# Optimization experiments

Measured on AMD Instinct MI355X. Metric: run time of the kernel, lower is better.

The kernel has to match this reference:

```python
import jax, jax.numpy as jnp
import numpy as np
from jax import lax

B, H, W, C = 4, 1024, 1024, 16


def setup_inputs() -> dict:
    key = jax.random.key(0)
    k1, k2 = jax.random.split(key)
    feat = jax.random.normal(k1, (B, H, W, C), dtype=jnp.float32)
    mask = jax.random.randint(k2, (B, H, W), 0, 2).astype(bool)
    return {"feat": feat, "mask": mask}


def _sum_pool(f, m):
    """Minkowski sum pooling, kernel 3, stride 2, dilation 1, dim 2.

    Output coord c exists iff any input coord in {2c, 2c+1}^2 is occupied
    (floor(coord/2) strided coordinate map). Output feature at c sums input
    features at 2c + {-1,0,1}^2 (3x3 window centered on the strided coord).
    """
    f = f * m[..., None].astype(f.dtype)  # zero features at empty coords
    # 3x3 sum window, stride 2, pad 1 -> output spatial dims H//2, W//2
    out = lax.reduce_window(
        f, jnp.zeros((), f.dtype), lax.add,
        window_dimensions=(1, 3, 3, 1),
        window_strides=(1, 2, 2, 1),
        padding=((0, 0), (1, 1), (1, 1), (0, 0)),
    )
    b, h, w = m.shape
    m2 = m.reshape(b, h // 2, 2, w // 2, 2).any(axis=(2, 4))  # strided coord map
    out = out * m2[..., None].astype(out.dtype)  # keep only occupied outputs
    return out, m2


def reference(feat, mask):
    c1, m1 = _sum_pool(feat, mask)
    c2, m2 = _sum_pool(c1, m1)
    c3, m3 = _sum_pool(c2, m2)
    return (c2, c3)
```

## Files before the change

kernel.cpp:

```cpp
#include <hip/hip_runtime.h>


constexpr int Hh = 1024, Ww = 1024;
constexpr int TW3 = 16, TH3 = 8;
constexpr int NU = 4 * TW3 + 3;
constexpr int NV = 2 * TW3 + 1;
constexpr int NY = TW3;
constexpr int NTH = 320;

#define BARRIER_LDS() asm volatile("s_waitcnt lgkmcnt(0)\ns_barrier" ::: "memory")

__device__ inline float4 add3(const float4& a, const float4& b, const float4& c) {
    return make_float4(a.x + b.x + c.x, a.y + b.y + c.y,
                       a.z + b.z + c.z, a.w + b.w + c.w);
}

__global__ __launch_bounds__(NTH) void fused3(
    const float* __restrict__ featp, const int* __restrict__ maskp,
    float4* __restrict__ c2o, float4* __restrict__ c3o)
{
    const int j = blockIdx.x;
    const int k = blockIdx.y;
    const int b = blockIdx.z;
    const int P0 = TW3 * j, Q0 = TH3 * k;
    const int F0 = 8 * P0 - 7;
    const int T0 = 8 * Q0 - 7;

    const int tid = threadIdx.x;
    const int c4 = tid & 3;
    const int u  = tid >> 2;
    const bool aAct = tid < NU * 4;
    const bool vAct = tid < NV * 4;
    const bool yAct = tid < NY * 4;

    __shared__ float4 c1m[2][NU][5];
    __shared__ float4 c2mS[2][NV][5];
    __shared__ unsigned char m1L[2][NU];
    __shared__ unsigned char m2L[2][NV];

    const float4* feat4 = reinterpret_cast<const float4*>(featp);
    const float4 z4 = make_float4(0.f, 0.f, 0.f, 0.f);

    auto ldMask = [&](int t, int* mm) {
#pragma unroll
        for (int dw = 0; dw < 3; ++dw) mm[dw] = 0;
        if (aAct && (unsigned)t < (unsigned)Hh) {
            const int base = (b * Hh + t) * Ww;
#pragma unroll
            for (int dw = 0; dw < 3; ++dw) {
                const int fcol = F0 + 2 * u + dw;
                if ((unsigned)fcol < (unsigned)Ww) mm[dw] = maskp[base + fcol];
            }
        }
    };
    auto ldFeat = [&](int t, const int* mm, float4* ff) {
#pragma unroll
        for (int dw = 0; dw < 3; ++dw) ff[dw] = z4;
        if (aAct && (unsigned)t < (unsigned)Hh) {
            const size_t base = (size_t)(b * Hh + t) * Ww;
#pragma unroll
            for (int dw = 0; dw < 3; ++dw) {
                const int fcol = F0 + 2 * u + dw;
                if (mm[dw])
                    ff[dw] = feat4[(base + fcol) * 4 + c4];
            }
        }
    };

    int mc[3], mn[3], mn2[3];
    float4 fcu[3], fn[3];
    ldMask(T0, mc);
    ldFeat(T0, mc, fcu);
    ldMask(T0 + 1, mn);

    float4 h0 = z4, h1 = z4;
    int mpPrev = 0;
    float4 r2h0 = z4, r2h1 = z4;
    float4 r3h0 = z4, r3h1 = z4;
    int m2save = 0, m3save = 0;

    for (int tt = 0; tt <= 70; ++tt) {
        const int t = T0 + tt;
        if (tt <= 68) ldMask(t + 2, mn2);
        else { mn2[0] = mn2[1] = mn2[2] = 0; }
        if (tt <= 69) ldFeat(t + 1, mn, fn);
        else { fn[0] = fn[1] = fn[2] = z4; }

        const float4 hc = add3(fcu[0], fcu[1], fcu[2]);
        const int mpCur = mc[1] | mc[2];

        if (t & 1) {
            const int s = (t - 1) >> 1;
            const int sb = s & 1;
            if (aAct) {
                const int m1 = mpPrev | mpCur;
                float4 cv = z4;
                if (m1) cv = add3(h0, h1, hc);
                c1m[sb][u][c4] = cv;
                if (c4 == 0) m1L[sb][u] = (unsigned char)(m1 ? 1 : 0);
            }
            BARRIER_LDS();
            float4 r2c = z4; int m2 = 0;
            if (vAct) {
                const float4 a0 = c1m[sb][2 * u + 0][c4];
                const float4 a1 = c1m[sb][2 * u + 1][c4];
                const float4 a2 = c1m[sb][2 * u + 2][c4];
                r2c = add3(a0, a1, a2);
                const int m2p = m1L[sb][2 * u + 1] | m1L[sb][2 * u + 2];
                if (s & 1) m2 = m2save | m2p; else m2save = m2p;
            }
            if ((t & 3) == 3) {
                const int r = (t - 3) >> 2;
                const int rb = r & 1;
                if (vAct) {
                    float4 c2v = z4;
                    if (m2) c2v = add3(r2h0, r2h1, r2c);
                    if (r >= 2 * Q0 && u >= 1) {
                        const int col = 2 * P0 - 1 + u;
                        c2o[((size_t)((b * 256 + r) * 256 + col)) * 4 + c4] = c2v;
                    }
                    c2mS[rb][u][c4] = c2v;
                    if (c4 == 0) m2L[rb][u] = (unsigned char)(m2 ? 1 : 0);
                }
                BARRIER_LDS();
                float4 r3c = z4; int m3 = 0;
                if (yAct) {
                    const float4 b0 = c2mS[rb][2 * u + 0][c4];
                    const float4 b1 = c2mS[rb][2 * u + 1][c4];
                    const float4 b2 = c2mS[rb][2 * u + 2][c4];
                    r3c = add3(b0, b1, b2);
                    const int m3p = m2L[rb][2 * u + 1] | m2L[rb][2 * u + 2];
                    if (r & 1) m3 = m3save | m3p; else m3save = m3p;
                }
                if ((t & 7) == 7) {
                    const int q = (t - 7) >> 3;
                    if (yAct && q >= Q0) {
                        float4 c3v = z4;
                        if (m3) c3v = add3(r3h0, r3h1, r3c);
                        c3o[((size_t)((b * 128 + q) * 128 + P0 + u)) * 4 + c4] = c3v;
                    }
                }
                r3h0 = r3h1; r3h1 = r3c;
            }
            r2h0 = r2h1; r2h1 = r2c;
        }

        h0 = h1; h1 = hc;
        mpPrev = mpCur;
        fcu[0] = fn[0]; fcu[1] = fn[1]; fcu[2] = fn[2];
        mc[0] = mn[0]; mc[1] = mn[1]; mc[2] = mn[2];
        mn[0] = mn2[0]; mn[1] = mn2[1]; mn[2] = mn2[2];
    }
}

extern "C" void kernel_launch(void* const* d_in, const int* in_sizes, int n_in,
                              void* d_out, int out_size, void* d_ws, size_t ws_size,
                              hipStream_t stream)
{
    const float* feat = (const float*)d_in[0];
    const int*   mask = (const int*)d_in[1];
    float4* c2 = (float4*)d_out;
    float4* c3 = c2 + (size_t)4 * 256 * 256 * 4;

    dim3 grid(Ww / (8 * TW3) , Hh / (8 * TH3) , 4);
    fused3<<<grid, NTH, 0, stream>>>(feat, mask, c2, c3);
}
```

Baseline: 65.26 us.

## Deepen feature/mask prefetch, halve tile height, use nontemporal output stores

Feature loads now run two rows ahead and mask loads four rows ahead, so more global loads are in flight per thread to hide latency. Tile height TH3 drops from 8 to 4, which doubles the grid to give more blocks and better occupancy. The cost is a larger halo overlap: each block streams 38 input rows for 32 useful ones instead of 70 for 64. Output stores to c2/c3 use nontemporal hints so they bypass cache retention, and the extra prefetch registers raise register pressure.

```diff
diff --git a/kernel.cpp b/kernel.cpp
--- a/kernel.cpp
+++ b/kernel.cpp
@@ -2,17 +2,24 @@
 
 
 constexpr int Hh = 1024, Ww = 1024;
-constexpr int TW3 = 16, TH3 = 8;
+constexpr int TW3 = 16, TH3 = 4;
 constexpr int NU = 4 * TW3 + 3;
 constexpr int NV = 2 * TW3 + 1;
 constexpr int NY = TW3;
 constexpr int NTH = 320;
+constexpr int TTMAX = 8 * TH3 + 6;
 
 #define BARRIER_LDS() asm volatile("s_waitcnt lgkmcnt(0)\ns_barrier" ::: "memory")
+
+typedef float f4_t __attribute__((ext_vector_type(4)));
 
 __device__ inline float4 add3(const float4& a, const float4& b, const float4& c) {
     return make_float4(a.x + b.x + c.x, a.y + b.y + c.y,
                        a.z + b.z + c.z, a.w + b.w + c.w);
+}
+__device__ inline void st_nt(float4* p, const float4& v) {
+    __builtin_nontemporal_store(*reinterpret_cast<const f4_t*>(&v),
+                                reinterpret_cast<f4_t*>(p));
 }
 
 __global__ __launch_bounds__(NTH) void fused3(
@@ -67,11 +74,14 @@
         }
     };
 
-    int mc[3], mn[3], mn2[3];
-    float4 fcu[3], fn[3];
-    ldMask(T0, mc);
-    ldFeat(T0, mc, fcu);
+    int mc[3], mn[3], mn2[3], mn3[3], mn4[3];
+    float4 fcu[3], fn[3], fn2[3];
+    ldMask(T0 + 0, mc);
     ldMask(T0 + 1, mn);
+    ldMask(T0 + 2, mn2);
+    ldMask(T0 + 3, mn3);
+    ldFeat(T0 + 0, mc, fcu);
+    ldFeat(T0 + 1, mn, fn);
 
     float4 h0 = z4, h1 = z4;
     int mpPrev = 0;
@@ -79,12 +89,12 @@
     float4 r3h0 = z4, r3h1 = z4;
     int m2save = 0, m3save = 0;
 
-    for (int tt = 0; tt <= 70; ++tt) {
+    for (int tt = 0; tt <= TTMAX; ++tt) {
         const int t = T0 + tt;
-        if (tt <= 68) ldMask(t + 2, mn2);
-        else { mn2[0] = mn2[1] = mn2[2] = 0; }
-        if (tt <= 69) ldFeat(t + 1, mn, fn);
-        else { fn[0] = fn[1] = fn[2] = z4; }
+        if (tt + 4 <= TTMAX) ldMask(t + 4, mn4);
+        else { mn4[0] = mn4[1] = mn4[2] = 0; }
+        if (tt + 2 <= TTMAX) ldFeat(t + 2, mn2, fn2);
+        else { fn2[0] = fn2[1] = fn2[2] = z4; }
 
         const float4 hc = add3(fcu[0], fcu[1], fcu[2]);
         const int mpCur = mc[1] | mc[2];
@@ -117,7 +127,7 @@
                     if (m2) c2v = add3(r2h0, r2h1, r2c);
                     if (r >= 2 * Q0 && u >= 1) {
                         const int col = 2 * P0 - 1 + u;
-                        c2o[((size_t)((b * 256 + r) * 256 + col)) * 4 + c4] = c2v;
+                        st_nt(&c2o[((size_t)((b * 256 + r) * 256 + col)) * 4 + c4], c2v);
                     }
                     c2mS[rb][u][c4] = c2v;
                     if (c4 == 0) m2L[rb][u] = (unsigned char)(m2 ? 1 : 0);
@@ -137,7 +147,7 @@
                     if (yAct && q >= Q0) {
                         float4 c3v = z4;
                         if (m3) c3v = add3(r3h0, r3h1, r3c);
-                        c3o[((size_t)((b * 128 + q) * 128 + P0 + u)) * 4 + c4] = c3v;
+                        st_nt(&c3o[((size_t)((b * 128 + q) * 128 + P0 + u)) * 4 + c4], c3v);
                     }
                 }
                 r3h0 = r3h1; r3h1 = r3c;
@@ -147,9 +157,12 @@
 
         h0 = h1; h1 = hc;
         mpPrev = mpCur;
-        fcu[0] = fn[0]; fcu[1] = fn[1]; fcu[2] = fn[2];
-        mc[0] = mn[0]; mc[1] = mn[1]; mc[2] = mn[2];
-        mn[0] = mn2[0]; mn[1] = mn2[1]; mn[2] = mn2[2];
+        fcu[0] = fn[0];  fcu[1] = fn[1];  fcu[2] = fn[2];
+        fn[0] = fn2[0];  fn[1] = fn2[1];  fn[2] = fn2[2];
+        mc[0] = mn[0];   mc[1] = mn[1];   mc[2] = mn[2];
+        mn[0] = mn2[0];  mn[1] = mn2[1];  mn[2] = mn2[2];
+        mn2[0] = mn3[0]; mn2[1] = mn3[1]; mn2[2] = mn3[2];
+        mn3[0] = mn4[0]; mn3[1] = mn4[1]; mn3[2] = mn4[2];
     }
 }
 
```

New measurement: 99.61 us. +52.6%, slower.

## Restructure row loop to process two input rows per iteration with deeper prefetch

Applied to the files above, without the earlier changes.

The main loop now advances over level-1 output rows, handling two input rows per iteration, instead of one input row with odd/even branching. Feature loads for the next two rows and mask loads for the two rows after that are issued before the LDS barrier, so more memory latency overlaps with the reduction work. The level-2 shared buffers drop their double buffering. This removes per-row branch overhead and a loop trip per pair, but uses more registers for the deeper prefetch, which could lower occupancy.

```diff
diff --git a/kernel.cpp b/kernel.cpp
--- a/kernel.cpp
+++ b/kernel.cpp
@@ -7,6 +7,7 @@
 constexpr int NV = 2 * TW3 + 1;
 constexpr int NY = TW3;
 constexpr int NTH = 320;
+constexpr int NS = 4 * TH3 + 3;
 
 #define BARRIER_LDS() asm volatile("s_waitcnt lgkmcnt(0)\ns_barrier" ::: "memory")
 
@@ -24,7 +25,7 @@
     const int b = blockIdx.z;
     const int P0 = TW3 * j, Q0 = TH3 * k;
     const int F0 = 8 * P0 - 7;
-    const int T0 = 8 * Q0 - 7;
+    const int S0 = 4 * Q0 - 3;
 
     const int tid = threadIdx.x;
     const int c4 = tid & 3;
@@ -34,122 +35,124 @@
     const bool yAct = tid < NY * 4;
 
     __shared__ float4 c1m[2][NU][5];
-    __shared__ float4 c2mS[2][NV][5];
+    __shared__ float4 c2mS[NV][5];
     __shared__ unsigned char m1L[2][NU];
-    __shared__ unsigned char m2L[2][NV];
+    __shared__ unsigned char m2L[NV];
 
     const float4* feat4 = reinterpret_cast<const float4*>(featp);
     const float4 z4 = make_float4(0.f, 0.f, 0.f, 0.f);
 
-    auto ldMask = [&](int t, int* mm) {
-#pragma unroll
-        for (int dw = 0; dw < 3; ++dw) mm[dw] = 0;
+    auto ldMaskRow = [&](int t, int* mm) {
+        mm[0] = mm[1] = mm[2] = 0;
         if (aAct && (unsigned)t < (unsigned)Hh) {
             const int base = (b * Hh + t) * Ww;
 #pragma unroll
             for (int dw = 0; dw < 3; ++dw) {
-                const int fcol = F0 + 2 * u + dw;
-                if ((unsigned)fcol < (unsigned)Ww) mm[dw] = maskp[base + fcol];
+                const int fc = F0 + 2 * u + dw;
+                if ((unsigned)fc < (unsigned)Ww) mm[dw] = maskp[base + fc];
             }
         }
     };
-    auto ldFeat = [&](int t, const int* mm, float4* ff) {
-#pragma unroll
-        for (int dw = 0; dw < 3; ++dw) ff[dw] = z4;
+    auto ldFeatRow = [&](int t, const int* mm, float4* ff) {
+        ff[0] = ff[1] = ff[2] = z4;
         if (aAct && (unsigned)t < (unsigned)Hh) {
             const size_t base = (size_t)(b * Hh + t) * Ww;
 #pragma unroll
             for (int dw = 0; dw < 3; ++dw) {
-                const int fcol = F0 + 2 * u + dw;
                 if (mm[dw])
-                    ff[dw] = feat4[(base + fcol) * 4 + c4];
+                    ff[dw] = feat4[(base + (F0 + 2 * u + dw)) * 4 + c4];
             }
         }
     };
 
-    int mc[3], mn[3], mn2[3];
-    float4 fcu[3], fn[3];
-    ldMask(T0, mc);
-    ldFeat(T0, mc, fcu);
-    ldMask(T0 + 1, mn);
+    int   mA[6];
+    float4 ffA[6];
+    float4 h_prev;
+    int   mp_cur;
+    {
+        int mP[3], m0[6];
+        ldMaskRow(2 * S0 - 1, mP);
+        ldMaskRow(2 * S0,     m0);
+        ldMaskRow(2 * S0 + 1, m0 + 3);
+        ldMaskRow(2 * S0 + 2, mA);
+        ldMaskRow(2 * S0 + 3, mA + 3);
+        float4 fP[3];
+        ldFeatRow(2 * S0 - 1, mP, fP);
+        ldFeatRow(2 * S0,     m0, ffA);
+        ldFeatRow(2 * S0 + 1, m0 + 3, ffA + 3);
+        h_prev = add3(fP[0], fP[1], fP[2]);
+        mp_cur = m0[1] | m0[2] | m0[4] | m0[5];
+    }
 
-    float4 h0 = z4, h1 = z4;
-    int mpPrev = 0;
     float4 r2h0 = z4, r2h1 = z4;
     float4 r3h0 = z4, r3h1 = z4;
     int m2save = 0, m3save = 0;
 
-    for (int tt = 0; tt <= 70; ++tt) {
-        const int t = T0 + tt;
-        if (tt <= 68) ldMask(t + 2, mn2);
-        else { mn2[0] = mn2[1] = mn2[2] = 0; }
-        if (tt <= 69) ldFeat(t + 1, mn, fn);
-        else { fn[0] = fn[1] = fn[2] = z4; }
-
-        const float4 hc = add3(fcu[0], fcu[1], fcu[2]);
-        const int mpCur = mc[1] | mc[2];
-
-        if (t & 1) {
-            const int s = (t - 1) >> 1;
-            const int sb = s & 1;
-            if (aAct) {
-                const int m1 = mpPrev | mpCur;
-                float4 cv = z4;
-                if (m1) cv = add3(h0, h1, hc);
-                c1m[sb][u][c4] = cv;
-                if (c4 == 0) m1L[sb][u] = (unsigned char)(m1 ? 1 : 0);
+    for (int i = 0; i < NS; ++i) {
+        const int sb = i & 1;
+        const float4 hc_e = add3(ffA[0], ffA[1], ffA[2]);
+        const float4 hc_o = add3(ffA[3], ffA[4], ffA[5]);
+        if (aAct) {
+            float4 cv = z4;
+            if (mp_cur) cv = add3(h_prev, hc_e, hc_o);
+            c1m[sb][u][c4] = cv;
+            if (c4 == 0) m1L[sb][u] = (unsigned char)(mp_cur ? 1 : 0);
+        }
+        const float4 hp_new = hc_o;
+        const int mp_new = mA[1] | mA[2] | mA[4] | mA[5];
+        const int t2 = 2 * (S0 + i) + 2;
+        if (i + 1 < NS) {
+            ldFeatRow(t2,     mA,     ffA);
+            ldFeatRow(t2 + 1, mA + 3, ffA + 3);
+        }
+        if (i + 2 < NS) {
+            ldMaskRow(t2 + 2, mA);
+            ldMaskRow(t2 + 3, mA + 3);
+        }
+        BARRIER_LDS();
+        float4 r2c = z4; int m2p = 0;
+        if (vAct) {
+            const float4 a0 = c1m[sb][2 * u + 0][c4];
+            const float4 a1 = c1m[sb][2 * u + 1][c4];
+            const float4 a2 = c1m[sb][2 * u + 2][c4];
+            r2c = add3(a0, a1, a2);
+            m2p = m1L[sb][2 * u + 1] | m1L[sb][2 * u + 2];
+        }
+        if ((i & 1) == 0) {
+            const int r = 2 * Q0 - 2 + (i >> 1);
+            if (vAct) {
+                const int m2 = m2save | m2p;
+                float4 c2v = z4;
+                if (m2) c2v = add3(r2h0, r2h1, r2c);
+                if (i >= 4 && u >= 1)
+                    c2o[((size_t)((b * 256 + r) * 256 + (2 * P0 - 1 + u))) * 4 + c4] = c2v;
+                c2mS[u][c4] = c2v;
+                if (c4 == 0) m2L[u] = (unsigned char)(m2 ? 1 : 0);
             }
             BARRIER_LDS();
-            float4 r2c = z4; int m2 = 0;
-            if (vAct) {
-                const float4 a0 = c1m[sb][2 * u + 0][c4];
-                const float4 a1 = c1m[sb][2 * u + 1][c4];
-                const float4 a2 = c1m[sb][2 * u + 2][c4];
-                r2c = add3(a0, a1, a2);
-                const int m2p = m1L[sb][2 * u + 1] | m1L[sb][2 * u + 2];
-                if (s & 1) m2 = m2save | m2p; else m2save = m2p;
+            float4 r3c = z4; int m3p = 0;
+            if (yAct) {
+                const float4 b0 = c2mS[2 * u + 0][c4];
+                const float4 b1 = c2mS[2 * u + 1][c4];
+                const float4 b2 = c2mS[2 * u + 2][c4];
+                r3c = add3(b0, b1, b2);
+                m3p = m2L[2 * u + 1] | m2L[2 * u + 2];
             }
-            if ((t & 3) == 3) {
-                const int r = (t - 3) >> 2;
-                const int rb = r & 1;
-                if (vAct) {
-                    float4 c2v = z4;
-                    if (m2) c2v = add3(r2h0, r2h1, r2c);
-                    if (r >= 2 * Q0 && u >= 1) {
-                        const int col = 2 * P0 - 1 + u;
-                        c2o[((size_t)((b * 256 + r) * 256 + col)) * 4 + c4] = c2v;
-                    }
-                    c2mS[rb][u][c4] = c2v;
-                    if (c4 == 0) m2L[rb][u] = (unsigned char)(m2 ? 1 : 0);
-                }
-                BARRIER_LDS();
-                float4 r3c = z4; int m3 = 0;
-                if (yAct) {
-                    const float4 b0 = c2mS[rb][2 * u + 0][c4];
-                    const float4 b1 = c2mS[rb][2 * u + 1][c4];
-                    const float4 b2 = c2mS[rb][2 * u + 2][c4];
-                    r3c = add3(b0, b1, b2);
-                    const int m3p = m2L[rb][2 * u + 1] | m2L[rb][2 * u + 2];
-                    if (r & 1) m3 = m3save | m3p; else m3save = m3p;
-                }
-                if ((t & 7) == 7) {
-                    const int q = (t - 7) >> 3;
-                    if (yAct && q >= Q0) {
-                        float4 c3v = z4;
-                        if (m3) c3v = add3(r3h0, r3h1, r3c);
-                        c3o[((size_t)((b * 128 + q) * 128 + P0 + u)) * 4 + c4] = c3v;
-                    }
-                }
-                r3h0 = r3h1; r3h1 = r3c;
+            if ((i & 2) == 0) {
+                m3save = m3p;
+            } else if (yAct && i >= 6) {
+                const int m3 = m3save | m3p;
+                float4 c3v = z4;
+                if (m3) c3v = add3(r3h0, r3h1, r3c);
+                const int q = Q0 + ((i - 6) >> 2);
+                c3o[((size_t)((b * 128 + q) * 128 + (P0 + u))) * 4 + c4] = c3v;
             }
-            r2h0 = r2h1; r2h1 = r2c;
+            r3h0 = r3h1; r3h1 = r3c;
+        } else {
+            m2save = m2p;
         }
-
-        h0 = h1; h1 = hc;
-        mpPrev = mpCur;
-        fcu[0] = fn[0]; fcu[1] = fn[1]; fcu[2] = fn[2];
-        mc[0] = mn[0]; mc[1] = mn[1]; mc[2] = mn[2];
-        mn[0] = mn2[0]; mn[1] = mn2[1]; mn[2] = mn2[2];
+        r2h0 = r2h1; r2h1 = r2c;
+        h_prev = hp_new; mp_cur = mp_new;
     }
 }
 
```

After: 60.83 us. 1.07x faster.
